# Kernel tuning notes

Hardware: AMD Instinct MI355X
Metric: run time of the kernel (lower is better)

Reference implementation:

```python
import jax, jax.numpy as jnp
import numpy as np

S, B, H = 1024, 4096, 8  # seq_len, batch, hidden (=input) size


def setup_inputs() -> dict:
    key = jax.random.key(0)
    k0, k1, k2, k3, k4 = jax.random.split(key, 5)
    scale = 1.0 / np.sqrt(H)  # matches torch uniform(-1/sqrt(H), 1/sqrt(H)) magnitude
    return {
        "input_": jax.random.normal(k0, (S, B, H), dtype=jnp.float32),
        "w_ih": jax.random.uniform(k1, (3 * H, H), jnp.float32, -scale, scale),
        "w_hh": jax.random.uniform(k2, (3 * H, H), jnp.float32, -scale, scale),
        "b_ih": jax.random.uniform(k3, (3 * H,), jnp.float32, -scale, scale),
        "b_hh": jax.random.uniform(k4, (3 * H,), jnp.float32, -scale, scale),
    }


def _gru_seq(input_, w_ih, w_hh, b_ih, b_hh):
    # Precompute input-side gate projections for all timesteps in one GEMM:
    # (S, B, 3H); gate order in PyTorch GRU is r, z, n.
    xg = jnp.einsum("sbi,gi->sbg", input_, w_ih) + b_ih
    h0 = jnp.zeros((input_.shape[1], w_hh.shape[1]), dtype=input_.dtype)

    def step(h, xg_t):
        hg = h @ w_hh.T + b_hh                      # (B, 3H)
        xr, xz, xn = jnp.split(xg_t, 3, axis=-1)
        hr, hz, hn = jnp.split(hg, 3, axis=-1)
        r = jax.nn.sigmoid(xr + hr)
        z = jax.nn.sigmoid(xz + hz)
        n = jnp.tanh(xn + r * hn)
        h_new = (1.0 - z) * n + z * h
        return h_new, h_new

    h_last, outputs = jax.lax.scan(step, h0, xg)
    return outputs, h_last[None]  # (S, B, H), (1, B, H) like torch GRU


def reference(input_, w_ih, w_hh, b_ih, b_hh):
    return _gru_seq(input_, w_ih, w_hh, b_ih, b_hh)
```

## Files before the change

kernel.cpp:

```cpp
#include <hip/hip_runtime.h>

#define SS 1024
#define BB 4096
#define HH 8
#define XSTRIDE (BB * HH)

typedef float f32x2 __attribute__((ext_vector_type(2)));

__device__ __forceinline__ int dpp_x1(int v) { return __builtin_amdgcn_mov_dpp(v, 0xB1, 0xF, 0xF, true); }
__device__ __forceinline__ int dpp_x2(int v) { return __builtin_amdgcn_mov_dpp(v, 0x4E, 0xF, 0xF, true); }
__device__ __forceinline__ int dpp_x7(int v) { return __builtin_amdgcn_mov_dpp(v, 0x141, 0xF, 0xF, true); }

__device__ __constant__ int MK_[8] = {0, 1, 2, 3, 7, 6, 5, 4};

#define ALOADD(DST, PTR) asm volatile("global_load_dword %0, %1, off" : "=v"(DST) : "v"(PTR))

#define WAITV(N) do {                                                                  \
    asm volatile("s_waitcnt vmcnt(" #N ")" ::: "memory");                              \
    __builtin_amdgcn_sched_barrier(0);                                                 \
} while (0)

#define BFLY8(SRC, DV) do {                                                            \
    const int b0_ = __float_as_int(SRC);                                               \
    const int b1_ = dpp_x1(b0_);                                                       \
    const int b2_ = dpp_x2(b0_);                                                       \
    const int b3_ = dpp_x2(b1_);                                                       \
    const int b4_ = dpp_x7(b0_);                                                       \
    const int b5_ = dpp_x7(b1_);                                                       \
    const int b6_ = dpp_x7(b2_);                                                       \
    const int b7_ = dpp_x7(b3_);                                                       \
    DV[0] = (f32x2){(SRC), __int_as_float(b1_)};                                       \
    DV[1] = (f32x2){__int_as_float(b2_), __int_as_float(b3_)};                         \
    DV[2] = (f32x2){__int_as_float(b4_), __int_as_float(b5_)};                         \
    DV[3] = (f32x2){__int_as_float(b6_), __int_as_float(b7_)};                         \
} while (0)

#define XFULL(BUF, V) do {                                                             \
    f32x2 xv_[4];                                                                      \
    BFLY8(BUF[V], xv_);                                                                \
    f32x2 sr_ = {bias_r, 0.0f}, sz_ = {bias_z, 0.0f}, sn_ = {bni_s, 0.0f};             \
    _Pragma("unroll")                                                                  \
    for (int p_ = 0; p_ < 4; ++p_) {                                                   \
        sr_ = __builtin_elementwise_fma(xv_[p_], wri[p_], sr_);                        \
        sz_ = __builtin_elementwise_fma(xv_[p_], wzi[p_], sz_);                        \
        sn_ = __builtin_elementwise_fma(xv_[p_], wni[p_], sn_);                        \
    }                                                                                  \
    xr[(V)] = sr_.x + sr_.y; xz[(V)] = sz_.x + sz_.y; xn[(V)] = sn_.x + sn_.y;         \
} while (0)

#define GROUP(BUF, SBASE) do {                                                         \
    XFULL(BUF, 0);                                                                     \
    XFULL(BUF, 1);                                                                     \
    _Pragma("unroll")                                                                  \
    for (int u = 0; u < 8; ++u) {                                                      \
                                \
        f32x2 hr2 = {xr[u], 0.0f}, hz2 = {xz[u], 0.0f}, hn2 = {bnh_s, 0.0f};           \
        _Pragma("unroll")                                                              \
        for (int p_ = 0; p_ < 4; ++p_) {                                               \
            hr2 = __builtin_elementwise_fma(hv2[p_], wrh[p_], hr2);                    \
            hz2 = __builtin_elementwise_fma(hv2[p_], wzh[p_], hz2);                    \
            hn2 = __builtin_elementwise_fma(hv2[p_], wnh[p_], hn2);                    \
        }                                                                              \
        const float srr = hr2.x + hr2.y;                                               \
        const float szz = hz2.x + hz2.y;                                               \
        const float snn = hn2.x + hn2.y;                                               \
        const bool W = (u + 2 < 8);                                                    \
        f32x2 xv_[4], sr_, sz_, sn_;                                                   \
        if (W) {                        \
            BFLY8(BUF[u + 2], xv_);                                                    \
            sr_ = (f32x2){bias_r, 0.0f}; sz_ = (f32x2){bias_z, 0.0f};                  \
            sn_ = (f32x2){bni_s, 0.0f};                                                \
            sr_ = __builtin_elementwise_fma(xv_[0], wri[0], sr_);                      \
            sz_ = __builtin_elementwise_fma(xv_[0], wzi[0], sz_);                      \
            sn_ = __builtin_elementwise_fma(xv_[0], wni[0], sn_);                      \
            sr_ = __builtin_elementwise_fma(xv_[1], wri[1], sr_);                      \
            sz_ = __builtin_elementwise_fma(xv_[1], wzi[1], sz_);                      \
            sn_ = __builtin_elementwise_fma(xv_[1], wni[1], sn_);                      \
        }                                                                              \
        const float er = __builtin_amdgcn_exp2f(srr);                                  \
        const float ez = __builtin_amdgcn_exp2f(szz);                                  \
        if (W) {                                     \
            sr_ = __builtin_elementwise_fma(xv_[2], wri[2], sr_);                      \
            sz_ = __builtin_elementwise_fma(xv_[2], wzi[2], sz_);                      \
            sn_ = __builtin_elementwise_fma(xv_[2], wni[2], sn_);                      \
            sr_ = __builtin_elementwise_fma(xv_[3], wri[3], sr_);                      \
            sz_ = __builtin_elementwise_fma(xv_[3], wzi[3], sz_);                      \
            sn_ = __builtin_elementwise_fma(xv_[3], wni[3], sn_);                      \
        }                                                                              \
        const float r_ = __builtin_amdgcn_rcpf(1.0f + er);                             \
        const float z_ = __builtin_amdgcn_rcpf(1.0f + ez);                             \
        if (W) {                                                    \
            xr[u + 2] = sr_.x + sr_.y;                                                 \
            xz[u + 2] = sz_.x + sz_.y;                                                 \
            xn[u + 2] = sn_.x + sn_.y;                                                 \
        }                                                                              \
        const float en = __builtin_amdgcn_exp2f(fmaf(r_, snn, xn[u]));                 \
        const float n_ = fmaf(-2.0f, __builtin_amdgcn_rcpf(1.0f + en), 1.0f);          \
        h = n_ + z_ * (h - n_);                                                        \
        const int hb_ = __float_as_int(h);                                             \
        const int t1_ = dpp_x1(hb_);                                                   \
        const int t2_ = dpp_x2(hb_);                                                   \
        const int t3_ = dpp_x2(t1_);                                                   \
        const int t4_ = dpp_x7(hb_);                                                   \
        const int t5_ = dpp_x7(t1_);                                                   \
        const int t6_ = dpp_x7(t2_);                                                   \
        const int t7_ = dpp_x7(t3_);                                                   \
        hv2[0] = (f32x2){h, __int_as_float(t1_)};                                      \
        hv2[1] = (f32x2){__int_as_float(t2_), __int_as_float(t3_)};                    \
        hv2[2] = (f32x2){__int_as_float(t4_), __int_as_float(t5_)};                    \
        hv2[3] = (f32x2){__int_as_float(t6_), __int_as_float(t7_)};                    \
        __builtin_nontemporal_store(h, &op[(size_t)((SBASE) + u) * XSTRIDE]);          \
    }                                                                                  \
} while (0)

#define LOADG(BUF, GRP) do {                                                           \
    const float* bp_ = xq + (size_t)(GRP) * 8 * XSTRIDE;                               \
    _Pragma("unroll")                                                                  \
    for (int u_ = 0; u_ < 8; ++u_) ALOADD(BUF[u_], bp_ + (size_t)u_ * XSTRIDE);        \
} while (0)

__global__ __launch_bounds__(64, 1) void gru_kernel(
    const float* __restrict__ x,
    const float* __restrict__ w_ih,
    const float* __restrict__ w_hh,
    const float* __restrict__ b_ih,
    const float* __restrict__ b_hh,
    float* __restrict__ out)
{
    const int lane = threadIdx.x;
    const int j = lane & 7;

    const float SR = -1.4426950408889634f;
    const float SN = 2.8853900817779268f;

    f32x2 wri[4], wzi[4], wni[4], wrh[4], wzh[4], wnh[4];
    #pragma unroll
    for (int p = 0; p < 4; ++p) {
        const int c0 = j ^ MK_[2 * p], c1 = j ^ MK_[2 * p + 1];
        wri[p] = (f32x2){SR * w_ih[j * 8 + c0],        SR * w_ih[j * 8 + c1]};
        wzi[p] = (f32x2){SR * w_ih[(8 + j) * 8 + c0],  SR * w_ih[(8 + j) * 8 + c1]};
        wni[p] = (f32x2){SN * w_ih[(16 + j) * 8 + c0], SN * w_ih[(16 + j) * 8 + c1]};
        wrh[p] = (f32x2){SR * w_hh[j * 8 + c0],        SR * w_hh[j * 8 + c1]};
        wzh[p] = (f32x2){SR * w_hh[(8 + j) * 8 + c0],  SR * w_hh[(8 + j) * 8 + c1]};
        wnh[p] = (f32x2){SN * w_hh[(16 + j) * 8 + c0], SN * w_hh[(16 + j) * 8 + c1]};
    }
    const float bias_r = SR * (b_ih[j] + b_hh[j]);
    const float bias_z = SR * (b_ih[8 + j] + b_hh[8 + j]);
    const float bni_s  = SN * b_ih[16 + j];
    const float bnh_s  = SN * b_hh[16 + j];

    const float* xq = x + (blockIdx.x << 6) + lane;
    float* op = out + (blockIdx.x << 6) + lane;
    float* hlast = out + (size_t)SS * BB * HH + (blockIdx.x << 6) + lane;

    float xA[8], xB[8];

    LOADG(xA, 0);
    LOADG(xB, 1);
    WAITV(8);

    float h = 0.0f;
    f32x2 hv2[4] = {{0,0},{0,0},{0,0},{0,0}};
    float xr[8], xz[8], xn[8];

    for (int g = 0; g < 124; g += 2) {
        GROUP(xA, g * 8);
        LOADG(xA, g + 2);
        WAITV(16);
        GROUP(xB, (g + 1) * 8);
        LOADG(xB, g + 3);
        WAITV(16);
    }
    GROUP(xA, 992);  LOADG(xA, 126); WAITV(16);
    GROUP(xB, 1000); LOADG(xB, 127); WAITV(16);
    GROUP(xA, 1008); WAITV(8);
    GROUP(xB, 1016);

    *hlast = h;
}

extern "C" void kernel_launch(void* const* d_in, const int* in_sizes, int n_in,
                              void* d_out, int out_size, void* d_ws, size_t ws_size,
                              hipStream_t stream) {
    const float* x    = (const float*)d_in[0];
    const float* w_ih = (const float*)d_in[1];
    const float* w_hh = (const float*)d_in[2];
    const float* b_ih = (const float*)d_in[3];
    const float* b_hh = (const float*)d_in[4];
    float* out = (float*)d_out;
    gru_kernel<<<BB / 8, 64, 0, stream>>>(x, w_ih, w_hh, b_ih, b_hh, out);
}
```

Measured before the change: 144.9 us.

## Interleave two independent batch chains per wavefront to hide recurrence latency

Each 64-lane block now processes two independent groups of 8 batch rows (P and Q), interleaving their GRU recurrences so the dependent DPP/exp/rcp chain of one can overlap with the other. The grid is halved to 256 blocks and the loads use an offset:256 second load per pointer, with groups reduced from 8 to 4 timesteps. This trades occupancy and CU coverage (256 waves instead of 512, one per block) for more instruction-level parallelism within each wave.

```diff
diff --git a/kernel.cpp b/kernel.cpp
--- a/kernel.cpp
+++ b/kernel.cpp
@@ -4,6 +4,7 @@
 #define BB 4096
 #define HH 8
 #define XSTRIDE (BB * HH)
+#define NG 256
 
 typedef float f32x2 __attribute__((ext_vector_type(2)));
 
@@ -13,7 +14,8 @@
 
 __device__ __constant__ int MK_[8] = {0, 1, 2, 3, 7, 6, 5, 4};
 
-#define ALOADD(DST, PTR) asm volatile("global_load_dword %0, %1, off" : "=v"(DST) : "v"(PTR))
+#define ALOADP(DST, PTR) asm volatile("global_load_dword %0, %1, off" : "=v"(DST) : "v"(PTR))
+#define ALOADQ(DST, PTR) asm volatile("global_load_dword %0, %1, off offset:256" : "=v"(DST) : "v"(PTR))
 
 #define WAITV(N) do {                                                                  \
     asm volatile("s_waitcnt vmcnt(" #N ")" ::: "memory");                              \
@@ -35,88 +37,132 @@
     DV[3] = (f32x2){__int_as_float(b6_), __int_as_float(b7_)};                         \
 } while (0)
 
-#define XFULL(BUF, V) do {                                                             \
-    f32x2 xv_[4];                                                                      \
-    BFLY8(BUF[V], xv_);                                                                \
-    f32x2 sr_ = {bias_r, 0.0f}, sz_ = {bias_z, 0.0f}, sn_ = {bni_s, 0.0f};             \
+#define BFLYH(C) do {                                                                  \
+    const int hb_ = __float_as_int(C##h);                                              \
+    const int t1_ = dpp_x1(hb_);                                                       \
+    const int t2_ = dpp_x2(hb_);                                                       \
+    const int t3_ = dpp_x2(t1_);                                                       \
+    const int t4_ = dpp_x7(hb_);                                                       \
+    const int t5_ = dpp_x7(t1_);                                                       \
+    const int t6_ = dpp_x7(t2_);                                                       \
+    const int t7_ = dpp_x7(t3_);                                                       \
+    C##hv[0] = (f32x2){C##h, __int_as_float(t1_)};                                     \
+    C##hv[1] = (f32x2){__int_as_float(t2_), __int_as_float(t3_)};                      \
+    C##hv[2] = (f32x2){__int_as_float(t4_), __int_as_float(t5_)};                      \
+    C##hv[3] = (f32x2){__int_as_float(t6_), __int_as_float(t7_)};                      \
+} while (0)
+
+#define XFULL2(PB, QB, V) do {                                                         \
+    f32x2 pxv[4], qxv[4];                                                              \
+    BFLY8(PB[V], pxv);                                                                 \
+    BFLY8(QB[V], qxv);                                                                 \
+    f32x2 psr = {bias_r, 0.0f}, qsr = {bias_r, 0.0f};                                  \
+    f32x2 psz = {bias_z, 0.0f}, qsz = {bias_z, 0.0f};                                  \
+    f32x2 psn = {bni_s, 0.0f},  qsn = {bni_s, 0.0f};                                   \
     _Pragma("unroll")                                                                  \
     for (int p_ = 0; p_ < 4; ++p_) {                                                   \
-        sr_ = __builtin_elementwise_fma(xv_[p_], wri[p_], sr_);                        \
-        sz_ = __builtin_elementwise_fma(xv_[p_], wzi[p_], sz_);                        \
-        sn_ = __builtin_elementwise_fma(xv_[p_], wni[p_], sn_);                        \
+        psr = __builtin_elementwise_fma(pxv[p_], wri[p_], psr);                        \
+        qsr = __builtin_elementwise_fma(qxv[p_], wri[p_], qsr);                        \
+        psz = __builtin_elementwise_fma(pxv[p_], wzi[p_], psz);                        \
+        qsz = __builtin_elementwise_fma(qxv[p_], wzi[p_], qsz);                        \
+        psn = __builtin_elementwise_fma(pxv[p_], wni[p_], psn);                        \
+        qsn = __builtin_elementwise_fma(qxv[p_], wni[p_], qsn);                        \
     }                                                                                  \
-    xr[(V)] = sr_.x + sr_.y; xz[(V)] = sz_.x + sz_.y; xn[(V)] = sn_.x + sn_.y;         \
-} while (0)
-
-#define GROUP(BUF, SBASE) do {                                                         \
-    XFULL(BUF, 0);                                                                     \
-    XFULL(BUF, 1);                                                                     \
+    Pxr[(V)] = psr.x + psr.y; Qxr[(V)] = qsr.x + qsr.y;                                \
+    Pxz[(V)] = psz.x + psz.y; Qxz[(V)] = qsz.x + qsz.y;                                \
+    Pxn[(V)] = psn.x + psn.y; Qxn[(V)] = qsn.x + qsn.y;                                \
+} while (0)
+
+#define GROUP(PB, QB) do {                                                             \
+    XFULL2(PB, QB, 0);                                                                 \
+    XFULL2(PB, QB, 1);                                                                 \
     _Pragma("unroll")                                                                  \
-    for (int u = 0; u < 8; ++u) {                                                      \
-                                \
-        f32x2 hr2 = {xr[u], 0.0f}, hz2 = {xz[u], 0.0f}, hn2 = {bnh_s, 0.0f};           \
+    for (int u = 0; u < 4; ++u) {                                                      \
+                        \
+        f32x2 Pr2 = {Pxr[u], 0.0f}, Qr2 = {Qxr[u], 0.0f};                              \
+        f32x2 Pz2 = {Pxz[u], 0.0f}, Qz2 = {Qxz[u], 0.0f};                              \
+        f32x2 Pn2 = {bnh_s, 0.0f},  Qn2 = {bnh_s, 0.0f};                               \
         _Pragma("unroll")                                                              \
         for (int p_ = 0; p_ < 4; ++p_) {                                               \
-            hr2 = __builtin_elementwise_fma(hv2[p_], wrh[p_], hr2);                    \
-            hz2 = __builtin_elementwise_fma(hv2[p_], wzh[p_], hz2);                    \
-            hn2 = __builtin_elementwise_fma(hv2[p_], wnh[p_], hn2);                    \
-        }                                                                              \
-        const float srr = hr2.x + hr2.y;                                               \
-        const float szz = hz2.x + hz2.y;                                               \
-        const float snn = hn2.x + hn2.y;                                               \
-        const bool W = (u + 2 < 8);                                                    \
-        f32x2 xv_[4], sr_, sz_, sn_;                                                   \
-        if (W) {                        \
-            BFLY8(BUF[u + 2], xv_);                                                    \
-            sr_ = (f32x2){bias_r, 0.0f}; sz_ = (f32x2){bias_z, 0.0f};                  \
-            sn_ = (f32x2){bni_s, 0.0f};                                                \
-            sr_ = __builtin_elementwise_fma(xv_[0], wri[0], sr_);                      \
-            sz_ = __builtin_elementwise_fma(xv_[0], wzi[0], sz_);                      \
-            sn_ = __builtin_elementwise_fma(xv_[0], wni[0], sn_);                      \
-            sr_ = __builtin_elementwise_fma(xv_[1], wri[1], sr_);                      \
-            sz_ = __builtin_elementwise_fma(xv_[1], wzi[1], sz_);                      \
-            sn_ = __builtin_elementwise_fma(xv_[1], wni[1], sn_);                      \
-        }                                                                              \
-        const float er = __builtin_amdgcn_exp2f(srr);                                  \
-        const float ez = __builtin_amdgcn_exp2f(szz);                                  \
-        if (W) {                                     \
-            sr_ = __builtin_elementwise_fma(xv_[2], wri[2], sr_);                      \
-            sz_ = __builtin_elementwise_fma(xv_[2], wzi[2], sz_);                      \
-            sn_ = __builtin_elementwise_fma(xv_[2], wni[2], sn_);                      \
-            sr_ = __builtin_elementwise_fma(xv_[3], wri[3], sr_);                      \
-            sz_ = __builtin_elementwise_fma(xv_[3], wzi[3], sz_);                      \
-            sn_ = __builtin_elementwise_fma(xv_[3], wni[3], sn_);                      \
-        }                                                                              \
-        const float r_ = __builtin_amdgcn_rcpf(1.0f + er);                             \
-        const float z_ = __builtin_amdgcn_rcpf(1.0f + ez);                             \
-        if (W) {                                                    \
-            xr[u + 2] = sr_.x + sr_.y;                                                 \
-            xz[u + 2] = sz_.x + sz_.y;                                                 \
-            xn[u + 2] = sn_.x + sn_.y;                                                 \
-        }                                                                              \
-        const float en = __builtin_amdgcn_exp2f(fmaf(r_, snn, xn[u]));                 \
-        const float n_ = fmaf(-2.0f, __builtin_amdgcn_rcpf(1.0f + en), 1.0f);          \
-        h = n_ + z_ * (h - n_);                                                        \
-        const int hb_ = __float_as_int(h);                                             \
-        const int t1_ = dpp_x1(hb_);                                                   \
-        const int t2_ = dpp_x2(hb_);                                                   \
-        const int t3_ = dpp_x2(t1_);                                                   \
-        const int t4_ = dpp_x7(hb_);                                                   \
-        const int t5_ = dpp_x7(t1_);                                                   \
-        const int t6_ = dpp_x7(t2_);                                                   \
-        const int t7_ = dpp_x7(t3_);                                                   \
-        hv2[0] = (f32x2){h, __int_as_float(t1_)};                                      \
-        hv2[1] = (f32x2){__int_as_float(t2_), __int_as_float(t3_)};                    \
-        hv2[2] = (f32x2){__int_as_float(t4_), __int_as_float(t5_)};                    \
-        hv2[3] = (f32x2){__int_as_float(t6_), __int_as_float(t7_)};                    \
-        __builtin_nontemporal_store(h, &op[(size_t)((SBASE) + u) * XSTRIDE]);          \
+            Pr2 = __builtin_elementwise_fma(Phv[p_], wrh[p_], Pr2);                    \
+            Qr2 = __builtin_elementwise_fma(Qhv[p_], wrh[p_], Qr2);                    \
+            Pz2 = __builtin_elementwise_fma(Phv[p_], wzh[p_], Pz2);                    \
+            Qz2 = __builtin_elementwise_fma(Qhv[p_], wzh[p_], Qz2);                    \
+            Pn2 = __builtin_elementwise_fma(Phv[p_], wnh[p_], Pn2);                    \
+            Qn2 = __builtin_elementwise_fma(Qhv[p_], wnh[p_], Qn2);                    \
+        }                                                                              \
+        const float Psr = Pr2.x + Pr2.y, Qsr = Qr2.x + Qr2.y;                          \
+        const float Psz = Pz2.x + Pz2.y, Qsz = Qz2.x + Qz2.y;                          \
+        const float Psn = Pn2.x + Pn2.y, Qsn = Qn2.x + Qn2.y;                          \
+        const bool W = (u + 2 < 4);                                                    \
+        f32x2 pxv[4], qxv[4], psr_, psz_, psn_, qsr_, qsz_, qsn_;                      \
+        if (W) {               \
+            BFLY8(PB[u + 2], pxv);                                                     \
+            BFLY8(QB[u + 2], qxv);                                                     \
+            psr_ = (f32x2){bias_r, 0.0f}; qsr_ = (f32x2){bias_r, 0.0f};                \
+            psz_ = (f32x2){bias_z, 0.0f}; qsz_ = (f32x2){bias_z, 0.0f};                \
+            psn_ = (f32x2){bni_s, 0.0f};  qsn_ = (f32x2){bni_s, 0.0f};                 \
+            psr_ = __builtin_elementwise_fma(pxv[0], wri[0], psr_);                    \
+            qsr_ = __builtin_elementwise_fma(qxv[0], wri[0], qsr_);                    \
+            psz_ = __builtin_elementwise_fma(pxv[0], wzi[0], psz_);                    \
+            qsz_ = __builtin_elementwise_fma(qxv[0], wzi[0], qsz_);                    \
+            psn_ = __builtin_elementwise_fma(pxv[0], wni[0], psn_);                    \
+            qsn_ = __builtin_elementwise_fma(qxv[0], wni[0], qsn_);                    \
+            psr_ = __builtin_elementwise_fma(pxv[1], wri[1], psr_);                    \
+            qsr_ = __builtin_elementwise_fma(qxv[1], wri[1], qsr_);                    \
+            psz_ = __builtin_elementwise_fma(pxv[1], wzi[1], psz_);                    \
+            qsz_ = __builtin_elementwise_fma(qxv[1], wzi[1], qsz_);                    \
+            psn_ = __builtin_elementwise_fma(pxv[1], wni[1], psn_);                    \
+            qsn_ = __builtin_elementwise_fma(qxv[1], wni[1], qsn_);                    \
+        }                                                                              \
+        const float PEr = __builtin_amdgcn_exp2f(Psr);                                 \
+        const float QEr = __builtin_amdgcn_exp2f(Qsr);                                 \
+        const float PEz = __builtin_amdgcn_exp2f(Psz);                                 \
+        const float QEz = __builtin_amdgcn_exp2f(Qsz);                                 \
+        if (W) {                              \
+            psr_ = __builtin_elementwise_fma(pxv[2], wri[2], psr_);                    \
+            qsr_ = __builtin_elementwise_fma(qxv[2], wri[2], qsr_);                    \
+            psz_ = __builtin_elementwise_fma(pxv[2], wzi[2], psz_);                    \
+            qsz_ = __builtin_elementwise_fma(qxv[2], wzi[2], qsz_);                    \
+            psn_ = __builtin_elementwise_fma(pxv[2], wni[2], psn_);                    \
+            qsn_ = __builtin_elementwise_fma(qxv[2], wni[2], qsn_);                    \
+            psr_ = __builtin_elementwise_fma(pxv[3], wri[3], psr_);                    \
+            qsr_ = __builtin_elementwise_fma(qxv[3], wri[3], qsr_);                    \
+            psz_ = __builtin_elementwise_fma(pxv[3], wzi[3], psz_);                    \
+            qsz_ = __builtin_elementwise_fma(qxv[3], wzi[3], qsz_);                    \
+            psn_ = __builtin_elementwise_fma(pxv[3], wni[3], psn_);                    \
+            qsn_ = __builtin_elementwise_fma(qxv[3], wni[3], qsn_);                    \
+        }                                                                              \
+        const float Pr_ = __builtin_amdgcn_rcpf(1.0f + PEr);                           \
+        const float Qr_ = __builtin_amdgcn_rcpf(1.0f + QEr);                           \
+        const float Pz_ = __builtin_amdgcn_rcpf(1.0f + PEz);                           \
+        const float Qz_ = __builtin_amdgcn_rcpf(1.0f + QEz);                           \
+        if (W) {                                              \
+            Pxr[u + 2] = psr_.x + psr_.y; Qxr[u + 2] = qsr_.x + qsr_.y;                \
+            Pxz[u + 2] = psz_.x + psz_.y; Qxz[u + 2] = qsz_.x + qsz_.y;                \
+            Pxn[u + 2] = psn_.x + psn_.y; Qxn[u + 2] = qsn_.x + qsn_.y;                \
+        }                                                                              \
+        const float PEn = __builtin_amdgcn_exp2f(fmaf(Pr_, Psn, Pxn[u]));              \
+        const float QEn = __builtin_amdgcn_exp2f(fmaf(Qr_, Qsn, Qxn[u]));              \
+        const float Pn_ = fmaf(-2.0f, __builtin_amdgcn_rcpf(1.0f + PEn), 1.0f);        \
+        const float Qn_ = fmaf(-2.0f, __builtin_amdgcn_rcpf(1.0f + QEn), 1.0f);        \
+        Ph = Pn_ + Pz_ * (Ph - Pn_);                                                   \
+        Qh = Qn_ + Qz_ * (Qh - Qn_);                                                   \
+        BFLYH(P);                                                                      \
+        BFLYH(Q);                                                                      \
+        __builtin_nontemporal_store(Ph, Pop + (size_t)u * XSTRIDE);                    \
+        __builtin_nontemporal_store(Qh, Pop + (size_t)u * XSTRIDE + 64);               \
     }                                                                                  \
-} while (0)
-
-#define LOADG(BUF, GRP) do {                                                           \
-    const float* bp_ = xq + (size_t)(GRP) * 8 * XSTRIDE;                               \
-    _Pragma("unroll")                                                                  \
-    for (int u_ = 0; u_ < 8; ++u_) ALOADD(BUF[u_], bp_ + (size_t)u_ * XSTRIDE);        \
+    Pop += 4 * (size_t)XSTRIDE;                                                        \
+} while (0)
+
+#define LOADG(PB, QB) do {                                                             \
+    ALOADP(PB[0], pa0); ALOADQ(QB[0], pa0);                                            \
+    ALOADP(PB[1], pa1); ALOADQ(QB[1], pa1);                                            \
+    ALOADP(PB[2], pa2); ALOADQ(QB[2], pa2);                                            \
+    ALOADP(PB[3], pa3); ALOADQ(QB[3], pa3);                                            \
+    pa0 += 4 * (size_t)XSTRIDE; pa1 += 4 * (size_t)XSTRIDE;                            \
+    pa2 += 4 * (size_t)XSTRIDE; pa3 += 4 * (size_t)XSTRIDE;                            \
 } while (0)
 
 __global__ __launch_bounds__(64, 1) void gru_kernel(
@@ -149,34 +195,41 @@
     const float bni_s  = SN * b_ih[16 + j];
     const float bnh_s  = SN * b_hh[16 + j];
 
-    const float* xq = x + (blockIdx.x << 6) + lane;
-    float* op = out + (blockIdx.x << 6) + lane;
-    float* hlast = out + (size_t)SS * BB * HH + (blockIdx.x << 6) + lane;
-
-    float xA[8], xB[8];
-
-    LOADG(xA, 0);
-    LOADG(xB, 1);
+    const float* xq = x + (blockIdx.x << 7) + lane;
+    float* Pop = out + (blockIdx.x << 7) + lane;
+
+    const float* pa0 = xq;
+    const float* pa1 = xq + (size_t)XSTRIDE;
+    const float* pa2 = xq + 2 * (size_t)XSTRIDE;
+    const float* pa3 = xq + 3 * (size_t)XSTRIDE;
+
+    float PxA[4], PxB[4], QxA[4], QxB[4];
+
+    LOADG(PxA, QxA);
+    LOADG(PxB, QxB);
     WAITV(8);
 
-    float h = 0.0f;
-    f32x2 hv2[4] = {{0,0},{0,0},{0,0},{0,0}};
-    float xr[8], xz[8], xn[8];
-
-    for (int g = 0; g < 124; g += 2) {
-        GROUP(xA, g * 8);
-        LOADG(xA, g + 2);
+    float Ph = 0.0f, Qh = 0.0f;
+    f32x2 Phv[4] = {{0,0},{0,0},{0,0},{0,0}};
+    f32x2 Qhv[4] = {{0,0},{0,0},{0,0},{0,0}};
+    float Pxr[4], Pxz[4], Pxn[4], Qxr[4], Qxz[4], Qxn[4];
+
+    for (int g = 0; g < NG - 4; g += 2) {
+        GROUP(PxA, QxA);
+        LOADG(PxA, QxA);
         WAITV(16);
-        GROUP(xB, (g + 1) * 8);
-        LOADG(xB, g + 3);
+        GROUP(PxB, QxB);
+        LOADG(PxB, QxB);
         WAITV(16);
     }
-    GROUP(xA, 992);  LOADG(xA, 126); WAITV(16);
-    GROUP(xB, 1000); LOADG(xB, 127); WAITV(16);
-    GROUP(xA, 1008); WAITV(8);
-    GROUP(xB, 1016);
-
-    *hlast = h;
+    GROUP(PxA, QxA); LOADG(PxA, QxA); WAITV(16);
+    GROUP(PxB, QxB); LOADG(PxB, QxB); WAITV(16);
+    GROUP(PxA, QxA); WAITV(8);
+    GROUP(PxB, QxB);
+
+    float* Phl = out + (size_t)SS * BB * HH + (blockIdx.x << 7) + lane;
+    *Phl = Ph;
+    *(Phl + 64) = Qh;
 }
 
 extern "C" void kernel_launch(void* const* d_in, const int* in_sizes, int n_in,
@@ -188,5 +241,5 @@
     const float* b_ih = (const float*)d_in[3];
     const float* b_hh = (const float*)d_in[4];
     float* out = (float*)d_out;
-    gru_kernel<<<BB / 8, 64, 0, stream>>>(x, w_ih, w_hh, b_ih, b_hh, out);
+    gru_kernel<<<BB / 16, 64, 0, stream>>>(x, w_ih, w_hh, b_ih, b_hh, out);
 }
```

Result: slower. 266.5 us (+83.9%).

## Split each hidden unit's 8-term dot product across two lanes per batch row

Applied to the files above, without the earlier changes.

Each batch row now uses 16 lanes instead of 8. Each lane computes a 4-term partial dot product for one hidden unit, and the two halves are combined with a row-shift DPP reduction. The grid doubles to BB/4 blocks, each wave covering 4 batch rows, and every lane holds one scalar h that it redistributes through a DPP pair. The aim is to shorten the serial per-step FMA chain and the DPP broadcast work on the recurrence critical path, paying for it with twice as many waves and duplicated stores and loads from the two halves.

```diff
diff --git a/kernel.cpp b/kernel.cpp
--- a/kernel.cpp
+++ b/kernel.cpp
@@ -5,13 +5,11 @@
 #define HH 8
 #define XSTRIDE (BB * HH)
 
-typedef float f32x2 __attribute__((ext_vector_type(2)));
-
 __device__ __forceinline__ int dpp_x1(int v) { return __builtin_amdgcn_mov_dpp(v, 0xB1, 0xF, 0xF, true); }
 __device__ __forceinline__ int dpp_x2(int v) { return __builtin_amdgcn_mov_dpp(v, 0x4E, 0xF, 0xF, true); }
+__device__ __forceinline__ int dpp_x3(int v) { return __builtin_amdgcn_mov_dpp(v, 0x1B, 0xF, 0xF, true); }
 __device__ __forceinline__ int dpp_x7(int v) { return __builtin_amdgcn_mov_dpp(v, 0x141, 0xF, 0xF, true); }
-
-__device__ __constant__ int MK_[8] = {0, 1, 2, 3, 7, 6, 5, 4};
+__device__ __forceinline__ int dpp_r8(int v) { return __builtin_amdgcn_mov_dpp(v, 0x128, 0xF, 0xF, true); }
 
 #define ALOADD(DST, PTR) asm volatile("global_load_dword %0, %1, off" : "=v"(DST) : "v"(PTR))
 
@@ -20,32 +18,22 @@
     __builtin_amdgcn_sched_barrier(0);                                                 \
 } while (0)
 
-#define BFLY8(SRC, DV) do {                                                            \
-    const int b0_ = __float_as_int(SRC);                                               \
-    const int b1_ = dpp_x1(b0_);                                                       \
-    const int b2_ = dpp_x2(b0_);                                                       \
-    const int b3_ = dpp_x2(b1_);                                                       \
-    const int b4_ = dpp_x7(b0_);                                                       \
-    const int b5_ = dpp_x7(b1_);                                                       \
-    const int b6_ = dpp_x7(b2_);                                                       \
-    const int b7_ = dpp_x7(b3_);                                                       \
-    DV[0] = (f32x2){(SRC), __int_as_float(b1_)};                                       \
-    DV[1] = (f32x2){__int_as_float(b2_), __int_as_float(b3_)};                         \
-    DV[2] = (f32x2){__int_as_float(b4_), __int_as_float(b5_)};                         \
-    DV[3] = (f32x2){__int_as_float(b6_), __int_as_float(b7_)};                         \
-} while (0)
-
 #define XFULL(BUF, V) do {                                                             \
-    f32x2 xv_[4];                                                                      \
-    BFLY8(BUF[V], xv_);                                                                \
-    f32x2 sr_ = {bias_r, 0.0f}, sz_ = {bias_z, 0.0f}, sn_ = {bni_s, 0.0f};             \
-    _Pragma("unroll")                                                                  \
-    for (int p_ = 0; p_ < 4; ++p_) {                                                   \
-        sr_ = __builtin_elementwise_fma(xv_[p_], wri[p_], sr_);                        \
-        sz_ = __builtin_elementwise_fma(xv_[p_], wzi[p_], sz_);                        \
-        sn_ = __builtin_elementwise_fma(xv_[p_], wni[p_], sn_);                        \
-    }                                                                                  \
-    xr[(V)] = sr_.x + sr_.y; xz[(V)] = sz_.x + sz_.y; xn[(V)] = sn_.x + sn_.y;         \
+    const float va = BUF[V];                                                           \
+    const int vai = __float_as_int(va);                                                \
+    const float vb = __int_as_float(dpp_x1(vai));                                      \
+    const float vc = __int_as_float(dpp_x2(vai));                                      \
+    const float vd = __int_as_float(dpp_x3(vai));                                      \
+    float sr0 = fmaf(va, wri[0], bias_rx); sr0 = fmaf(vb, wri[1], sr0);                \
+    float sr1 = vc * wri[2];               sr1 = fmaf(vd, wri[3], sr1);                \
+    float sz0 = fmaf(va, wzi[0], bias_zx); sz0 = fmaf(vb, wzi[1], sz0);                \
+    float sz1 = vc * wzi[2];               sz1 = fmaf(vd, wzi[3], sz1);                \
+    float sn0 = fmaf(va, wni[0], bias_nx); sn0 = fmaf(vb, wni[1], sn0);                \
+    float sn1 = vc * wni[2];               sn1 = fmaf(vd, wni[3], sn1);                \
+    const float srt = sr0 + sr1, szt = sz0 + sz1, snt = sn0 + sn1;                     \
+    xr[V] = srt + __int_as_float(dpp_r8(__float_as_int(srt)));                         \
+    xz[V] = szt + __int_as_float(dpp_r8(__float_as_int(szt)));                         \
+    xn[V] = snt + __int_as_float(dpp_r8(__float_as_int(snt)));                         \
 } while (0)
 
 #define GROUP(BUF, SBASE) do {                                                         \
@@ -53,62 +41,59 @@
     XFULL(BUF, 1);                                                                     \
     _Pragma("unroll")                                                                  \
     for (int u = 0; u < 8; ++u) {                                                      \
-                                \
-        f32x2 hr2 = {xr[u], 0.0f}, hz2 = {xz[u], 0.0f}, hn2 = {bnh_s, 0.0f};           \
-        _Pragma("unroll")                                                              \
-        for (int p_ = 0; p_ < 4; ++p_) {                                               \
-            hr2 = __builtin_elementwise_fma(hv2[p_], wrh[p_], hr2);                    \
-            hz2 = __builtin_elementwise_fma(hv2[p_], wzh[p_], hz2);                    \
-            hn2 = __builtin_elementwise_fma(hv2[p_], wnh[p_], hn2);                    \
-        }                                                                              \
-        const float srr = hr2.x + hr2.y;                                               \
-        const float szz = hz2.x + hz2.y;                                               \
-        const float snn = hn2.x + hn2.y;                                               \
+                                        \
+        const int hvi = __float_as_int(hv);                                            \
+        const float ha = hv;                                                           \
+        const float hbv = __int_as_float(dpp_x1(hvi));                                 \
+        const float hc = __int_as_float(dpp_x2(hvi));                                  \
+        const float hd = __int_as_float(dpp_x3(hvi));                                  \
+        float pr0 = ha * wrh[0];               pr0 = fmaf(hbv, wrh[1], pr0);           \
+        float pr1 = hc * wrh[2];               pr1 = fmaf(hd, wrh[3], pr1);            \
+        float pz0 = ha * wzh[0];               pz0 = fmaf(hbv, wzh[1], pz0);           \
+        float pz1 = hc * wzh[2];               pz1 = fmaf(hd, wzh[3], pz1);            \
+        float pn0 = fmaf(ha, wnh[0], bias_nh); pn0 = fmaf(hbv, wnh[1], pn0);           \
+        float pn1 = hc * wnh[2];               pn1 = fmaf(hd, wnh[3], pn1);            \
+        const float prt = pr0 + pr1, pzt = pz0 + pz1, pnt = pn0 + pn1;                 \
+        const float srr = xr[u] + (prt + __int_as_float(dpp_r8(__float_as_int(prt)))); \
+        const float szz = xz[u] + (pzt + __int_as_float(dpp_r8(__float_as_int(pzt)))); \
+        const float snn = pnt + __int_as_float(dpp_r8(__float_as_int(pnt)));           \
         const bool W = (u + 2 < 8);                                                    \
-        f32x2 xv_[4], sr_, sz_, sn_;                                                   \
-        if (W) {                        \
-            BFLY8(BUF[u + 2], xv_);                                                    \
-            sr_ = (f32x2){bias_r, 0.0f}; sz_ = (f32x2){bias_z, 0.0f};                  \
-            sn_ = (f32x2){bni_s, 0.0f};                                                \
-            sr_ = __builtin_elementwise_fma(xv_[0], wri[0], sr_);                      \
-            sz_ = __builtin_elementwise_fma(xv_[0], wzi[0], sz_);                      \
-            sn_ = __builtin_elementwise_fma(xv_[0], wni[0], sn_);                      \
-            sr_ = __builtin_elementwise_fma(xv_[1], wri[1], sr_);                      \
-            sz_ = __builtin_elementwise_fma(xv_[1], wzi[1], sz_);                      \
-            sn_ = __builtin_elementwise_fma(xv_[1], wni[1], sn_);                      \
+        float wsr0, wsr1, wsz0, wsz1, wsn0, wsn1;                                      \
+        float wvc, wvd;                                                                \
+        if (W) {                    \
+            const float va2 = BUF[u + 2];                                              \
+            const int va2i = __float_as_int(va2);                                      \
+            const float vb2 = __int_as_float(dpp_x1(va2i));                            \
+            wvc = __int_as_float(dpp_x2(va2i));                                        \
+            wvd = __int_as_float(dpp_x3(va2i));                                        \
+            wsr0 = fmaf(va2, wri[0], bias_rx); wsr0 = fmaf(vb2, wri[1], wsr0);         \
+            wsz0 = fmaf(va2, wzi[0], bias_zx); wsz0 = fmaf(vb2, wzi[1], wsz0);         \
+            wsn0 = fmaf(va2, wni[0], bias_nx); wsn0 = fmaf(vb2, wni[1], wsn0);         \
         }                                                                              \
         const float er = __builtin_amdgcn_exp2f(srr);                                  \
         const float ez = __builtin_amdgcn_exp2f(szz);                                  \
-        if (W) {                                     \
-            sr_ = __builtin_elementwise_fma(xv_[2], wri[2], sr_);                      \
-            sz_ = __builtin_elementwise_fma(xv_[2], wzi[2], sz_);                      \
-            sn_ = __builtin_elementwise_fma(xv_[2], wni[2], sn_);                      \
-            sr_ = __builtin_elementwise_fma(xv_[3], wri[3], sr_);                      \
-            sz_ = __builtin_elementwise_fma(xv_[3], wzi[3], sz_);                      \
-            sn_ = __builtin_elementwise_fma(xv_[3], wni[3], sn_);                      \
+        if (W) {                               \
+            wsr1 = wvc * wri[2]; wsr1 = fmaf(wvd, wri[3], wsr1);                       \
+            wsz1 = wvc * wzi[2]; wsz1 = fmaf(wvd, wzi[3], wsz1);                       \
+            wsn1 = wvc * wni[2]; wsn1 = fmaf(wvd, wni[3], wsn1);                       \
         }                                                                              \
         const float r_ = __builtin_amdgcn_rcpf(1.0f + er);                             \
         const float z_ = __builtin_amdgcn_rcpf(1.0f + ez);                             \
-        if (W) {                                                    \
-            xr[u + 2] = sr_.x + sr_.y;                                                 \
-            xz[u + 2] = sz_.x + sz_.y;                                                 \
-            xn[u + 2] = sn_.x + sn_.y;                                                 \
+        if (W) {                                  \
+            const float srt = wsr0 + wsr1, szt = wsz0 + wsz1, snt = wsn0 + wsn1;       \
+            xr[u + 2] = srt + __int_as_float(dpp_r8(__float_as_int(srt)));             \
+            xz[u + 2] = szt + __int_as_float(dpp_r8(__float_as_int(szt)));             \
+            xn[u + 2] = snt + __int_as_float(dpp_r8(__float_as_int(snt)));             \
         }                                                                              \
         const float en = __builtin_amdgcn_exp2f(fmaf(r_, snn, xn[u]));                 \
         const float n_ = fmaf(-2.0f, __builtin_amdgcn_rcpf(1.0f + en), 1.0f);          \
         h = n_ + z_ * (h - n_);                                                        \
-        const int hb_ = __float_as_int(h);                                             \
-        const int t1_ = dpp_x1(hb_);                                                   \
-        const int t2_ = dpp_x2(hb_);                                                   \
-        const int t3_ = dpp_x2(t1_);                                                   \
-        const int t4_ = dpp_x7(hb_);                                                   \
-        const int t5_ = dpp_x7(t1_);                                                   \
-        const int t6_ = dpp_x7(t2_);                                                   \
-        const int t7_ = dpp_x7(t3_);                                                   \
-        hv2[0] = (f32x2){h, __int_as_float(t1_)};                                      \
-        hv2[1] = (f32x2){__int_as_float(t2_), __int_as_float(t3_)};                    \
-        hv2[2] = (f32x2){__int_as_float(t4_), __int_as_float(t5_)};                    \
-        hv2[3] = (f32x2){__int_as_float(t6_), __int_as_float(t7_)};                    \
+            \
+        const int hbits = __float_as_int(h);                                           \
+        const int tA = dpp_x7(hbits);                                                  \
+        const int tB = dpp_x3(tA);                                                     \
+        hv = hiHalf ? __int_as_float(tB) : h;                                          \
+                          \
         __builtin_nontemporal_store(h, &op[(size_t)((SBASE) + u) * XSTRIDE]);          \
     }                                                                                  \
 } while (0)
@@ -128,30 +113,34 @@
     float* __restrict__ out)
 {
     const int lane = threadIdx.x;
-    const int j = lane & 7;
+    const int s16 = lane & 15;
+    const int j = s16 & 7;
+    const int half = s16 >> 3;
+    const bool hiHalf = (half != 0);
+    const int e0 = j ^ (half << 2);
 
     const float SR = -1.4426950408889634f;
     const float SN = 2.8853900817779268f;
 
-    f32x2 wri[4], wzi[4], wni[4], wrh[4], wzh[4], wnh[4];
+    float wri[4], wzi[4], wni[4], wrh[4], wzh[4], wnh[4];
     #pragma unroll
-    for (int p = 0; p < 4; ++p) {
-        const int c0 = j ^ MK_[2 * p], c1 = j ^ MK_[2 * p + 1];
-        wri[p] = (f32x2){SR * w_ih[j * 8 + c0],        SR * w_ih[j * 8 + c1]};
-        wzi[p] = (f32x2){SR * w_ih[(8 + j) * 8 + c0],  SR * w_ih[(8 + j) * 8 + c1]};
-        wni[p] = (f32x2){SN * w_ih[(16 + j) * 8 + c0], SN * w_ih[(16 + j) * 8 + c1]};
-        wrh[p] = (f32x2){SR * w_hh[j * 8 + c0],        SR * w_hh[j * 8 + c1]};
-        wzh[p] = (f32x2){SR * w_hh[(8 + j) * 8 + c0],  SR * w_hh[(8 + j) * 8 + c1]};
-        wnh[p] = (f32x2){SN * w_hh[(16 + j) * 8 + c0], SN * w_hh[(16 + j) * 8 + c1]};
+    for (int m = 0; m < 4; ++m) {
+        const int c = e0 ^ m;
+        wri[m] = SR * w_ih[j * 8 + c];
+        wzi[m] = SR * w_ih[(8 + j) * 8 + c];
+        wni[m] = SN * w_ih[(16 + j) * 8 + c];
+        wrh[m] = SR * w_hh[j * 8 + c];
+        wzh[m] = SR * w_hh[(8 + j) * 8 + c];
+        wnh[m] = SN * w_hh[(16 + j) * 8 + c];
     }
-    const float bias_r = SR * (b_ih[j] + b_hh[j]);
-    const float bias_z = SR * (b_ih[8 + j] + b_hh[8 + j]);
-    const float bni_s  = SN * b_ih[16 + j];
-    const float bnh_s  = SN * b_hh[16 + j];
+    const float bias_rx = hiHalf ? 0.0f : SR * (b_ih[j] + b_hh[j]);
+    const float bias_zx = hiHalf ? 0.0f : SR * (b_ih[8 + j] + b_hh[8 + j]);
+    const float bias_nx = hiHalf ? 0.0f : SN * b_ih[16 + j];
+    const float bias_nh = hiHalf ? 0.0f : SN * b_hh[16 + j];
 
-    const float* xq = x + (blockIdx.x << 6) + lane;
-    float* op = out + (blockIdx.x << 6) + lane;
-    float* hlast = out + (size_t)SS * BB * HH + (blockIdx.x << 6) + lane;
+    const float* xq = x + (blockIdx.x << 5) + ((lane >> 4) << 3) + e0;
+    float* op = out + (blockIdx.x << 5) + ((lane >> 4) << 3) + j;
+    float* hlast = out + (size_t)SS * BB * HH + (blockIdx.x << 5) + ((lane >> 4) << 3) + j;
 
     float xA[8], xB[8];
 
@@ -160,7 +149,7 @@
     WAITV(8);
 
     float h = 0.0f;
-    f32x2 hv2[4] = {{0,0},{0,0},{0,0},{0,0}};
+    float hv = 0.0f;
     float xr[8], xz[8], xn[8];
 
     for (int g = 0; g < 124; g += 2) {
@@ -188,5 +177,5 @@
     const float* b_ih = (const float*)d_in[3];
     const float* b_hh = (const float*)d_in[4];
     float* out = (float*)d_out;
-    gru_kernel<<<BB / 8, 64, 0, stream>>>(x, w_ih, w_hh, b_ih, b_hh, out);
+    gru_kernel<<<BB / 4, 64, 0, stream>>>(x, w_ih, w_hh, b_ih, b_hh, out);
 }
```

Result: faster. 137.5 us (-5.1%).
